# Optimization experiments

Measured on AMD Instinct MI355X. Metric: run time of the kernel, lower is better.

## Reference

```python
import jax, jax.numpy as jnp
import numpy as np

D_MODEL = 1024
H = 16
D_K = D_MODEL // H


def setup_inputs() -> dict:
    key = jax.random.key(0)
    ks = jax.random.split(key, 13)
    B, S = 4, 2048
    scale = 1.0 / np.sqrt(D_MODEL)
    inp = {
        "query": jax.random.normal(ks[0], (B, S, D_MODEL), jnp.float32),
        "key": jax.random.normal(ks[1], (B, S, D_MODEL), jnp.float32),
        "value": jax.random.normal(ks[2], (B, S, D_MODEL), jnp.float32),
        "mask": jax.random.randint(ks[3], (B, S, S), 0, 2, jnp.int32),
        "Wq": jax.random.normal(ks[4], (D_MODEL, D_MODEL), jnp.float32) * scale,
        "bq": jnp.zeros((D_MODEL,), jnp.float32),
        "Wk": jax.random.normal(ks[5], (D_MODEL, D_MODEL), jnp.float32) * scale,
        "bk": jnp.zeros((D_MODEL,), jnp.float32),
        "Wv": jax.random.normal(ks[6], (D_MODEL, D_MODEL), jnp.float32) * scale,
        "bv": jnp.zeros((D_MODEL,), jnp.float32),
        "Wo": jax.random.normal(ks[7], (D_MODEL, D_MODEL), jnp.float32) * scale,
        "bo": jnp.zeros((D_MODEL,), jnp.float32),
    }
    return inp


def _split_heads(x):
    # [B, S, D] -> [B, H, S, d_k]
    B, S, _ = x.shape
    return x.reshape(B, S, H, D_K).transpose(0, 2, 1, 3)


def reference(query, key, value, mask, Wq, bq, Wk, bk, Wv, bv, Wo, bo):
    B, S, _ = query.shape
    q = _split_heads(query @ Wq + bq)
    k = _split_heads(key @ Wk + bk)
    v = _split_heads(value @ Wv + bv)
    # scores: [B, H, S, S]
    scores = jnp.einsum("bhqd,bhkd->bhqk", q, k) / jnp.sqrt(jnp.float32(D_K))
    scores = jnp.where(mask[:, None, :, :] == 0, jnp.float32(-1e9), scores)
    prob = jax.nn.softmax(scores, axis=-1)
    out = jnp.einsum("bhqk,bhkd->bhqd", prob, v)
    out = out.transpose(0, 2, 1, 3).reshape(B, S, D_MODEL)
    return out @ Wo + bo
```

## Files before the change

### kernel.cpp

```cpp
#include <hip/hip_runtime.h>
#include <hip/hip_bf16.h>


typedef __bf16 bf16;
typedef __bf16 bf16x4 __attribute__((ext_vector_type(4)));
typedef __bf16 bf16x8 __attribute__((ext_vector_type(8)));
typedef float f32x4 __attribute__((ext_vector_type(4)));

__device__ __forceinline__ void gload_lds16(const void* g, void* l) {
  __builtin_amdgcn_global_load_lds(
      (__attribute__((address_space(1))) void*)g,
      (__attribute__((address_space(3))) void*)l, 16, 0, 0);
}

__global__ __launch_bounds__(256) void wt_kernel(const float* __restrict__ Wq,
                                                 const float* __restrict__ Wk,
                                                 const float* __restrict__ Wv,
                                                 const float* __restrict__ Wo,
                                                 bf16* __restrict__ wt) {
  __shared__ float tile[64][65];
  const int z = blockIdx.z;
  const float* W = (z == 0) ? Wq : (z == 1) ? Wk : (z == 2) ? Wv : Wo;
  bf16* out = wt + (size_t)z * 1048576;
  const int k0 = blockIdx.x * 64, n0 = blockIdx.y * 64;
  for (int e = threadIdx.x; e < 4096; e += 256) {
    int r = e >> 6, c = e & 63;
    tile[r][c] = W[(size_t)(k0 + r) * 1024 + n0 + c];
  }
  __syncthreads();
  for (int e = threadIdx.x; e < 4096; e += 256) {
    int r = e >> 6, c = e & 63;
    out[(size_t)(n0 + r) * 1024 + k0 + c] = (bf16)tile[c][r];
  }
}

__global__ __launch_bounds__(256) void maskpack_kernel(const int* __restrict__ mask,
                                                       unsigned long long* __restrict__ bits) {
  const int gid = blockIdx.x * 256 + threadIdx.x;
  const int word = gid >> 6;
  const int lane = threadIdx.x & 63;
  int v = mask[(size_t)word * 64 + lane];
  unsigned long long b = __ballot(v != 0);
  if (lane == 0) bits[word] = b;
}

template <int MODE>
__global__ __launch_bounds__(256) void gemm_kernel(const void* __restrict__ Aptr,
                                                   const bf16* __restrict__ Bt,
                                                   const float* __restrict__ bias,
                                                   void* __restrict__ Out) {
  __shared__ alignas(16) char smem[32768];
  char* As = smem;
  char* Bs = smem + 16384;
  const int t = threadIdx.x;
  const int w = t >> 6, l = t & 63;
  const int hi = l >> 4, lo = l & 15, l7 = l & 7;
  const int wr = w >> 1, wc = w & 1;
  const int row0 = blockIdx.x * 128;
  const int n0 = blockIdx.y * 128;

  const f32x4 fz = {0.f, 0.f, 0.f, 0.f};
  f32x4 acc[4][4];
#pragma unroll
  for (int mi = 0; mi < 4; ++mi)
#pragma unroll
    for (int ni = 0; ni < 4; ++ni) acc[mi][ni] = fz;

  for (int kt = 0; kt < 16; ++kt) {
    if constexpr (MODE < 3) {
      const float* A = (const float*)Aptr;
#pragma unroll
      for (int i = 0; i < 8; ++i) {
        int qq = i * 256 + t;
        int r = qq >> 4, q = qq & 15;
        f32x4 f = *(const f32x4*)(A + (size_t)(row0 + r) * 1024 + kt * 64 + q * 4);
        bf16x4 h = {(bf16)f[0], (bf16)f[1], (bf16)f[2], (bf16)f[3]};
        *(bf16x4*)(As + r * 128 + ((q * 8) ^ ((r & 7) << 4))) = h;
      }
    } else {
      const char* A = (const char*)Aptr;
#pragma unroll
      for (int i = 0; i < 4; ++i) {
        int c = i * 256 + t;
        int r = c >> 3, s = c & 7;
        gload_lds16(A + (size_t)(row0 + r) * 2048 + kt * 128 + ((s ^ (r & 7)) * 16),
                    As + (i * 256 + w * 64) * 16);
      }
    }
    {
      const char* Bb = (const char*)Bt;
#pragma unroll
      for (int i = 0; i < 4; ++i) {
        int c = i * 256 + t;
        int r = c >> 3, s = c & 7;
        gload_lds16(Bb + (size_t)(n0 + r) * 2048 + kt * 128 + ((s ^ (r & 7)) * 16),
                    Bs + (i * 256 + w * 64) * 16);
      }
    }
    __syncthreads();
#pragma unroll
    for (int kk = 0; kk < 2; ++kk) {
      bf16x8 af[4], bfr[4];
#pragma unroll
      for (int mi = 0; mi < 4; ++mi)
        af[mi] = *(const bf16x8*)(As + (wr * 64 + mi * 16 + lo) * 128 +
                                  ((kk * 64 + hi * 16) ^ (l7 << 4)));
#pragma unroll
      for (int ni = 0; ni < 4; ++ni)
        bfr[ni] = *(const bf16x8*)(Bs + (wc * 64 + ni * 16 + lo) * 128 +
                                   ((kk * 64 + hi * 16) ^ (l7 << 4)));
#pragma unroll
      for (int mi = 0; mi < 4; ++mi)
#pragma unroll
        for (int ni = 0; ni < 4; ++ni)
          acc[mi][ni] =
              __builtin_amdgcn_mfma_f32_16x16x32_bf16(af[mi], bfr[ni], acc[mi][ni], 0, 0, 0);
    }
    __syncthreads();
  }

#pragma unroll
  for (int mi = 0; mi < 4; ++mi)
#pragma unroll
    for (int ni = 0; ni < 4; ++ni) {
      int gcol = n0 + wc * 64 + ni * 16 + lo;
      float bv = bias[gcol];
#pragma unroll
      for (int j = 0; j < 4; ++j) {
        int grow = row0 + wr * 64 + mi * 16 + hi * 4 + j;
        float v = acc[mi][ni][j] + bv;
        if constexpr (MODE == 0) v *= 0.125f;
        if constexpr (MODE <= 1) {
          int b = grow >> 11, si = grow & 2047, h = gcol >> 6, d = gcol & 63;
          ((bf16*)Out)[((((size_t)b * 16 + h) * 2048 + si) << 6) + d] = (bf16)v;
        } else if constexpr (MODE == 2) {
          int b = grow >> 11, si = grow & 2047, h = gcol >> 6, d = gcol & 63;
          ((bf16*)Out)[((((size_t)b * 16 + h) * 64 + d) << 11) + si] = (bf16)v;
        } else {
          ((float*)Out)[(size_t)grow * 1024 + gcol] = v;
        }
      }
    }
}

__global__ __launch_bounds__(256) void attn_kernel(const char* __restrict__ qb,
                                                   const char* __restrict__ kb,
                                                   const char* __restrict__ vb,
                                                   const unsigned long long* __restrict__ mbits,
                                                   bf16* __restrict__ out) {
  __shared__ alignas(16) char smem[49152];
  const int t = threadIdx.x;
  const int w = t >> 6, l = t & 63;
  const int hi = l >> 4, lo = l & 15, l7 = l & 7;
  char* Ps = smem + 32768 + w * 4096;
  const int bh = blockIdx.x, b = bh >> 4, h = bh & 15;
  const int q0 = blockIdx.y * 128;
  const int qrow = q0 + w * 32 + lo;

  bf16x8 qf[2][2];
#pragma unroll
  for (int mi = 0; mi < 2; ++mi)
#pragma unroll
    for (int kk = 0; kk < 2; ++kk)
      qf[mi][kk] = *(const bf16x8*)(qb + ((size_t)(bh * 2048 + qrow + mi * 16) * 64 +
                                          kk * 32 + hi * 8) * 2);

  const f32x4 fz = {0.f, 0.f, 0.f, 0.f};
  f32x4 o[4][2];
  float mx[2] = {-3e38f, -3e38f}, ls[2] = {0.f, 0.f};
#pragma unroll
  for (int dj = 0; dj < 4; ++dj)
#pragma unroll
    for (int mi = 0; mi < 2; ++mi) o[dj][mi] = fz;

  for (int kt2 = 0; kt2 < 16; ++kt2) {
#pragma unroll
    for (int i = 0; i < 4; ++i) {
      int c = i * 256 + t;
      int kr = c >> 3, ks = c & 7;
      gload_lds16(kb + (size_t)(bh * 2048 + kt2 * 128 + kr) * 128 + ((ks ^ (kr & 7)) * 16),
                  smem + (i * 256 + w * 64) * 16);
      int vr = c >> 4, vs = c & 15;
      gload_lds16(vb + (size_t)(bh * 64 + vr) * 4096 + kt2 * 256 + ((vs ^ (vr & 7)) * 16),
                  smem + 16384 + (i * 256 + w * 64) * 16);
    }
    __syncthreads();

#pragma unroll
    for (int h2 = 0; h2 < 2; ++h2) {
      const char* Kb = smem + h2 * 8192;
      const char* Vb = smem + 16384;
      const int kt = kt2 * 2 + h2;

      unsigned long long mw[2];
#pragma unroll
      for (int mi = 0; mi < 2; ++mi)
        mw[mi] = mbits[(size_t)(b * 2048 + qrow + mi * 16) * 32 + kt];

      f32x4 sc[4][2];
#pragma unroll
      for (int ni = 0; ni < 4; ++ni)
#pragma unroll
        for (int mi = 0; mi < 2; ++mi) sc[ni][mi] = fz;
#pragma unroll
      for (int kk = 0; kk < 2; ++kk) {
        bf16x8 kf[4];
#pragma unroll
        for (int ni = 0; ni < 4; ++ni)
          kf[ni] =
              *(const bf16x8*)(Kb + (ni * 16 + lo) * 128 + ((kk * 64 + hi * 16) ^ (l7 << 4)));
#pragma unroll
        for (int ni = 0; ni < 4; ++ni)
#pragma unroll
          for (int mi = 0; mi < 2; ++mi)
            sc[ni][mi] =
                __builtin_amdgcn_mfma_f32_16x16x32_bf16(kf[ni], qf[mi][kk], sc[ni][mi], 0, 0, 0);
      }

#pragma unroll
      for (int mi = 0; mi < 2; ++mi) {
        float sv[4][4];
#pragma unroll
        for (int ni = 0; ni < 4; ++ni)
#pragma unroll
          for (int j = 0; j < 4; ++j)
            sv[ni][j] = ((mw[mi] >> (ni * 16 + hi * 4 + j)) & 1ull) ? sc[ni][mi][j] : -1e9f;
        float tm = sv[0][0];
#pragma unroll
        for (int ni = 0; ni < 4; ++ni)
#pragma unroll
          for (int j = 0; j < 4; ++j) tm = fmaxf(tm, sv[ni][j]);
        tm = fmaxf(tm, __shfl_xor(tm, 16));
        tm = fmaxf(tm, __shfl_xor(tm, 32));
        float mn = fmaxf(mx[mi], tm);
        float scal = __expf(mx[mi] - mn);
        float ps = 0.f;
        const int row = mi * 16 + lo;
#pragma unroll
        for (int ni = 0; ni < 4; ++ni) {
          float p0 = __expf(sv[ni][0] - mn), p1 = __expf(sv[ni][1] - mn);
          float p2 = __expf(sv[ni][2] - mn), p3 = __expf(sv[ni][3] - mn);
          ps += (p0 + p1) + (p2 + p3);
          bf16x4 hq = {(bf16)p0, (bf16)p1, (bf16)p2, (bf16)p3};
          *(bf16x4*)(Ps + row * 128 + ((ni * 32 + hi * 8) ^ ((row & 7) << 4))) = hq;
        }
        ps += __shfl_xor(ps, 16);
        ps += __shfl_xor(ps, 32);
        ls[mi] = ls[mi] * scal + ps;
        mx[mi] = mn;
#pragma unroll
        for (int dj = 0; dj < 4; ++dj) o[dj][mi] *= scal;
      }

#pragma unroll
      for (int kk = 0; kk < 2; ++kk) {
        bf16x8 pf[2], vf[4];
#pragma unroll
        for (int mi = 0; mi < 2; ++mi)
          pf[mi] =
              *(const bf16x8*)(Ps + (mi * 16 + lo) * 128 + ((kk * 64 + hi * 16) ^ (l7 << 4)));
#pragma unroll
        for (int dj = 0; dj < 4; ++dj)
          vf[dj] = *(const bf16x8*)(Vb + (dj * 16 + lo) * 256 +
                                    ((h2 * 128 + kk * 64 + hi * 16) ^ (l7 << 4)));
#pragma unroll
        for (int dj = 0; dj < 4; ++dj)
#pragma unroll
          for (int mi = 0; mi < 2; ++mi)
            o[dj][mi] =
                __builtin_amdgcn_mfma_f32_16x16x32_bf16(vf[dj], pf[mi], o[dj][mi], 0, 0, 0);
      }
    }
    __syncthreads();
  }

#pragma unroll
  for (int mi = 0; mi < 2; ++mi) {
    float inv = 1.f / ls[mi];
    size_t rbase = (size_t)((b << 11) + qrow + mi * 16) * 1024 + h * 64;
#pragma unroll
    for (int dj = 0; dj < 4; ++dj) {
      bf16x4 hv = {(bf16)(o[dj][mi][0] * inv), (bf16)(o[dj][mi][1] * inv),
                   (bf16)(o[dj][mi][2] * inv), (bf16)(o[dj][mi][3] * inv)};
      *(bf16x4*)(out + rbase + dj * 16 + hi * 4) = hv;
    }
  }
}

extern "C" void kernel_launch(void* const* d_in, const int* in_sizes, int n_in,
                              void* d_out, int out_size, void* d_ws, size_t ws_size,
                              hipStream_t stream) {
  const float* query = (const float*)d_in[0];
  const float* key_ = (const float*)d_in[1];
  const float* value = (const float*)d_in[2];
  const int* mask = (const int*)d_in[3];
  const float* Wq = (const float*)d_in[4];
  const float* bq = (const float*)d_in[5];
  const float* Wk = (const float*)d_in[6];
  const float* bk = (const float*)d_in[7];
  const float* Wv = (const float*)d_in[8];
  const float* bv = (const float*)d_in[9];
  const float* Wo = (const float*)d_in[10];
  const float* bo = (const float*)d_in[11];

  char* ws = (char*)d_ws;
  bf16* wt = (bf16*)ws;
  char* qbuf = ws + 8388608;
  char* kbuf = qbuf + 16777216;
  char* vbuf = kbuf + 16777216;
  char* abuf = vbuf + 16777216;
  unsigned long long* mbits = (unsigned long long*)(abuf + 16777216);

  wt_kernel<<<dim3(16, 16, 4), 256, 0, stream>>>(Wq, Wk, Wv, Wo, wt);
  maskpack_kernel<<<65536, 256, 0, stream>>>(mask, mbits);
  gemm_kernel<0><<<dim3(64, 8), 256, 0, stream>>>(query, wt, bq, qbuf);
  gemm_kernel<1><<<dim3(64, 8), 256, 0, stream>>>(key_, wt + 1048576, bk, kbuf);
  gemm_kernel<2><<<dim3(64, 8), 256, 0, stream>>>(value, wt + 2097152, bv, vbuf);
  attn_kernel<<<dim3(64, 16), 256, 0, stream>>>(qbuf, kbuf, vbuf, mbits, (bf16*)abuf);
  gemm_kernel<3><<<dim3(64, 8), 256, 0, stream>>>(abuf, wt + 3145728, bo, d_out);
}
```

Before: 326.5 us.

## Rewrite attention core with 32x32 MFMA, register-resident P, lazy rescale, exp2

The attention inner loop switches from 16x16x32 to 32x32x16 bf16 MFMA tiles, with one 32-row query tile per wave. Probabilities stay in registers via v_cvt_pk_bf16_f32 and v_permlane32_swap instead of a round trip through an LDS P buffer, which shrinks LDS use. Softmax folds log2(e) into the Q scale so it can use exp2, and the running-max rescale is skipped unless some row's max grows by more than 4 (in log2 units). s_setprio is added around the MFMA sections; the looser rescale threshold gives a bit more headroom for overflow and precision drift.

Result: faster. 296.1 us (-9.3%).

```diff
diff --git a/kernel.cpp b/kernel.cpp
--- a/kernel.cpp
+++ b/kernel.cpp
@@ -6,6 +6,8 @@
 typedef __bf16 bf16x4 __attribute__((ext_vector_type(4)));
 typedef __bf16 bf16x8 __attribute__((ext_vector_type(8)));
 typedef float f32x4 __attribute__((ext_vector_type(4)));
+typedef float f32x16 __attribute__((ext_vector_type(16)));
+typedef unsigned int uint;
 
 __device__ __forceinline__ void gload_lds16(const void* g, void* l) {
   __builtin_amdgcn_global_load_lds(
@@ -129,7 +131,7 @@
       for (int j = 0; j < 4; ++j) {
         int grow = row0 + wr * 64 + mi * 16 + hi * 4 + j;
         float v = acc[mi][ni][j] + bv;
-        if constexpr (MODE == 0) v *= 0.125f;
+        if constexpr (MODE == 0) v *= 0.18033688011112042f;
         if constexpr (MODE <= 1) {
           int b = grow >> 11, si = grow & 2047, h = gcol >> 6, d = gcol & 63;
           ((bf16*)Out)[((((size_t)b * 16 + h) * 2048 + si) << 6) + d] = (bf16)v;
@@ -148,30 +150,26 @@
                                                    const char* __restrict__ vb,
                                                    const unsigned long long* __restrict__ mbits,
                                                    bf16* __restrict__ out) {
-  __shared__ alignas(16) char smem[49152];
+  __shared__ alignas(16) char smem[32768];
   const int t = threadIdx.x;
   const int w = t >> 6, l = t & 63;
-  const int hi = l >> 4, lo = l & 15, l7 = l & 7;
-  char* Ps = smem + 32768 + w * 4096;
+  const int q31 = l & 31, hi = l >> 5;
   const int bh = blockIdx.x, b = bh >> 4, h = bh & 15;
   const int q0 = blockIdx.y * 128;
-  const int qrow = q0 + w * 32 + lo;
-
-  bf16x8 qf[2][2];
-#pragma unroll
-  for (int mi = 0; mi < 2; ++mi)
-#pragma unroll
-    for (int kk = 0; kk < 2; ++kk)
-      qf[mi][kk] = *(const bf16x8*)(qb + ((size_t)(bh * 2048 + qrow + mi * 16) * 64 +
-                                          kk * 32 + hi * 8) * 2);
-
-  const f32x4 fz = {0.f, 0.f, 0.f, 0.f};
-  f32x4 o[4][2];
-  float mx[2] = {-3e38f, -3e38f}, ls[2] = {0.f, 0.f};
-#pragma unroll
-  for (int dj = 0; dj < 4; ++dj)
-#pragma unroll
-    for (int mi = 0; mi < 2; ++mi) o[dj][mi] = fz;
+  const int qrow = q0 + w * 32 + q31;
+
+  bf16x8 qf[4];
+#pragma unroll
+  for (int kc = 0; kc < 4; ++kc)
+    qf[kc] = *(const bf16x8*)(qb + (size_t)(bh * 2048 + qrow) * 128 + kc * 32 + hi * 16);
+
+  const f32x16 fz16 = {0.f, 0.f, 0.f, 0.f, 0.f, 0.f, 0.f, 0.f,
+                       0.f, 0.f, 0.f, 0.f, 0.f, 0.f, 0.f, 0.f};
+  f32x16 o[2];
+  o[0] = fz16;
+  o[1] = fz16;
+  float mreg = -3e38f, ls = 0.f;
+  const unsigned long long* mrow = mbits + (size_t)(b * 2048 + qrow) * 32;
 
   for (int kt2 = 0; kt2 < 16; ++kt2) {
 #pragma unroll
@@ -188,103 +186,103 @@
 
 #pragma unroll
     for (int h2 = 0; h2 < 2; ++h2) {
-      const char* Kb = smem + h2 * 8192;
-      const char* Vb = smem + 16384;
       const int kt = kt2 * 2 + h2;
-
-      unsigned long long mw[2];
-#pragma unroll
-      for (int mi = 0; mi < 2; ++mi)
-        mw[mi] = mbits[(size_t)(b * 2048 + qrow + mi * 16) * 32 + kt];
-
-      f32x4 sc[4][2];
-#pragma unroll
-      for (int ni = 0; ni < 4; ++ni)
-#pragma unroll
-        for (int mi = 0; mi < 2; ++mi) sc[ni][mi] = fz;
-#pragma unroll
-      for (int kk = 0; kk < 2; ++kk) {
-        bf16x8 kf[4];
-#pragma unroll
-        for (int ni = 0; ni < 4; ++ni)
-          kf[ni] =
-              *(const bf16x8*)(Kb + (ni * 16 + lo) * 128 + ((kk * 64 + hi * 16) ^ (l7 << 4)));
-#pragma unroll
-        for (int ni = 0; ni < 4; ++ni)
-#pragma unroll
-          for (int mi = 0; mi < 2; ++mi)
-            sc[ni][mi] =
-                __builtin_amdgcn_mfma_f32_16x16x32_bf16(kf[ni], qf[mi][kk], sc[ni][mi], 0, 0, 0);
-      }
-
-#pragma unroll
-      for (int mi = 0; mi < 2; ++mi) {
-        float sv[4][4];
-#pragma unroll
-        for (int ni = 0; ni < 4; ++ni)
-#pragma unroll
-          for (int j = 0; j < 4; ++j)
-            sv[ni][j] = ((mw[mi] >> (ni * 16 + hi * 4 + j)) & 1ull) ? sc[ni][mi][j] : -1e9f;
-        float tm = sv[0][0];
-#pragma unroll
-        for (int ni = 0; ni < 4; ++ni)
-#pragma unroll
-          for (int j = 0; j < 4; ++j) tm = fmaxf(tm, sv[ni][j]);
-        tm = fmaxf(tm, __shfl_xor(tm, 16));
-        tm = fmaxf(tm, __shfl_xor(tm, 32));
-        float mn = fmaxf(mx[mi], tm);
-        float scal = __expf(mx[mi] - mn);
-        float ps = 0.f;
-        const int row = mi * 16 + lo;
-#pragma unroll
-        for (int ni = 0; ni < 4; ++ni) {
-          float p0 = __expf(sv[ni][0] - mn), p1 = __expf(sv[ni][1] - mn);
-          float p2 = __expf(sv[ni][2] - mn), p3 = __expf(sv[ni][3] - mn);
-          ps += (p0 + p1) + (p2 + p3);
-          bf16x4 hq = {(bf16)p0, (bf16)p1, (bf16)p2, (bf16)p3};
-          *(bf16x4*)(Ps + row * 128 + ((ni * 32 + hi * 8) ^ ((row & 7) << 4))) = hq;
+      const unsigned long long mw = mrow[kt];
+
+      f32x16 sc[2];
+      sc[0] = fz16;
+      sc[1] = fz16;
+      __builtin_amdgcn_s_setprio(1);
+#pragma unroll
+      for (int kc = 0; kc < 4; ++kc) {
+        bf16x8 kf0 = *(const bf16x8*)(smem + (h2 * 64 + q31) * 128 +
+                                      (((kc * 2 + hi) ^ (q31 & 7)) * 16));
+        bf16x8 kf1 = *(const bf16x8*)(smem + (h2 * 64 + 32 + q31) * 128 +
+                                      (((kc * 2 + hi) ^ (q31 & 7)) * 16));
+        sc[0] = __builtin_amdgcn_mfma_f32_32x32x16_bf16(kf0, qf[kc], sc[0], 0, 0, 0);
+        sc[1] = __builtin_amdgcn_mfma_f32_32x32x16_bf16(kf1, qf[kc], sc[1], 0, 0, 0);
+      }
+      __builtin_amdgcn_s_setprio(0);
+
+      float sv[2][16];
+      float tm = -3e38f;
+#pragma unroll
+      for (int n = 0; n < 2; ++n) {
+        uint m32 = (uint)(mw >> (n * 32 + 4 * hi));
+#pragma unroll
+        for (int r = 0; r < 16; ++r) {
+          const int bi = (r & 3) + 8 * (r >> 2);
+          float x = ((m32 >> bi) & 1u) ? sc[n][r] : -1e9f;
+          sv[n][r] = x;
+          tm = fmaxf(tm, x);
         }
-        ps += __shfl_xor(ps, 16);
-        ps += __shfl_xor(ps, 32);
-        ls[mi] = ls[mi] * scal + ps;
-        mx[mi] = mn;
-#pragma unroll
-        for (int dj = 0; dj < 4; ++dj) o[dj][mi] *= scal;
-      }
-
-#pragma unroll
-      for (int kk = 0; kk < 2; ++kk) {
-        bf16x8 pf[2], vf[4];
-#pragma unroll
-        for (int mi = 0; mi < 2; ++mi)
-          pf[mi] =
-              *(const bf16x8*)(Ps + (mi * 16 + lo) * 128 + ((kk * 64 + hi * 16) ^ (l7 << 4)));
-#pragma unroll
-        for (int dj = 0; dj < 4; ++dj)
-          vf[dj] = *(const bf16x8*)(Vb + (dj * 16 + lo) * 256 +
-                                    ((h2 * 128 + kk * 64 + hi * 16) ^ (l7 << 4)));
-#pragma unroll
-        for (int dj = 0; dj < 4; ++dj)
-#pragma unroll
-          for (int mi = 0; mi < 2; ++mi)
-            o[dj][mi] =
-                __builtin_amdgcn_mfma_f32_16x16x32_bf16(vf[dj], pf[mi], o[dj][mi], 0, 0, 0);
-      }
+      }
+      tm = fmaxf(tm, __shfl_xor(tm, 32));
+
+      if (!__all(tm - mreg <= 4.f)) {
+        float mn = fmaxf(mreg, tm);
+        float scal = __builtin_amdgcn_exp2f(mreg - mn);
+        ls *= scal;
+        o[0] *= scal;
+        o[1] *= scal;
+        mreg = mn;
+      }
+
+      uint wpk[2][8];
+#pragma unroll
+      for (int n = 0; n < 2; ++n)
+#pragma unroll
+        for (int r2 = 0; r2 < 8; ++r2) {
+          float p0 = __builtin_amdgcn_exp2f(sv[n][2 * r2] - mreg);
+          float p1 = __builtin_amdgcn_exp2f(sv[n][2 * r2 + 1] - mreg);
+          ls += p0 + p1;
+          uint pk;
+          asm("v_cvt_pk_bf16_f32 %0, %1, %2" : "=v"(pk) : "v"(p0), "v"(p1));
+          wpk[n][r2] = pk;
+        }
+
+      __builtin_amdgcn_s_setprio(1);
+#pragma unroll
+      for (int n = 0; n < 2; ++n)
+#pragma unroll
+        for (int c2 = 0; c2 < 2; ++c2) {
+          uint a0 = wpk[n][4 * c2], b0 = wpk[n][4 * c2 + 2];
+          uint a1 = wpk[n][4 * c2 + 1], b1 = wpk[n][4 * c2 + 3];
+          asm("v_permlane32_swap_b32 %0, %1" : "+v"(a0), "+v"(b0));
+          asm("v_permlane32_swap_b32 %0, %1" : "+v"(a1), "+v"(b1));
+          union {
+            uint u[4];
+            bf16x8 v;
+          } pf;
+          pf.u[0] = a0;
+          pf.u[1] = a1;
+          pf.u[2] = b0;
+          pf.u[3] = b1;
+          const int c = n * 2 + c2;
+          const int slot = (h2 * 8 + c * 2 + hi);
+          bf16x8 vf0 = *(const bf16x8*)(smem + 16384 + q31 * 256 +
+                                        ((slot ^ (q31 & 7)) * 16));
+          bf16x8 vf1 = *(const bf16x8*)(smem + 16384 + (32 + q31) * 256 +
+                                        ((slot ^ (q31 & 7)) * 16));
+          o[0] = __builtin_amdgcn_mfma_f32_32x32x16_bf16(vf0, pf.v, o[0], 0, 0, 0);
+          o[1] = __builtin_amdgcn_mfma_f32_32x32x16_bf16(vf1, pf.v, o[1], 0, 0, 0);
+        }
+      __builtin_amdgcn_s_setprio(0);
     }
     __syncthreads();
   }
 
-#pragma unroll
-  for (int mi = 0; mi < 2; ++mi) {
-    float inv = 1.f / ls[mi];
-    size_t rbase = (size_t)((b << 11) + qrow + mi * 16) * 1024 + h * 64;
-#pragma unroll
-    for (int dj = 0; dj < 4; ++dj) {
-      bf16x4 hv = {(bf16)(o[dj][mi][0] * inv), (bf16)(o[dj][mi][1] * inv),
-                   (bf16)(o[dj][mi][2] * inv), (bf16)(o[dj][mi][3] * inv)};
-      *(bf16x4*)(out + rbase + dj * 16 + hi * 4) = hv;
-    }
-  }
+  ls += __shfl_xor(ls, 32);
+  float inv = 1.f / ls;
+  size_t rbase = (size_t)((b << 11) + qrow) * 1024 + h * 64;
+#pragma unroll
+  for (int db = 0; db < 2; ++db)
+#pragma unroll
+    for (int g = 0; g < 4; ++g) {
+      bf16x4 hv = {(bf16)(o[db][4 * g] * inv), (bf16)(o[db][4 * g + 1] * inv),
+                   (bf16)(o[db][4 * g + 2] * inv), (bf16)(o[db][4 * g + 3] * inv)};
+      *(bf16x4*)(out + rbase + db * 32 + 8 * g + 4 * hi) = hv;
+    }
 }
 
 extern "C" void kernel_launch(void* const* d_in, const int* in_sizes, int n_in,
```
